# Optimization experiments

Measured on AMD Instinct MI355X. Metric: run time of the kernel, lower is better.

## Reference

```python
import jax, jax.numpy as jnp
import numpy as np

NV = 16384
NF = 32768
B = 4


def _build_laplacian(nv, nf, seed=0):
    # Faithful replication of the torch module's __init__ laplacian construction.
    rng = np.random.RandomState(seed)
    faces = rng.randint(0, nv, size=(nf, 3)).astype(np.int64)
    lap = np.zeros((nv, nv), dtype=np.float32)
    lap[faces[:, 0], faces[:, 1]] = -1
    lap[faces[:, 1], faces[:, 0]] = -1
    lap[faces[:, 1], faces[:, 2]] = -1
    lap[faces[:, 2], faces[:, 1]] = -1
    lap[faces[:, 2], faces[:, 0]] = -1
    lap[faces[:, 0], faces[:, 2]] = -1
    r, c = np.diag_indices(nv)
    lap[r, c] = -lap.sum(1)
    deg = lap[r, c]  # degree per vertex (>= 0)
    # vectorized version of: for i: if lap[i,i] > 0: lap[i,:] /= lap[i,i]
    scale = np.where(deg > 0, 1.0 / np.maximum(deg, 1.0), 1.0).astype(np.float32)
    lap = lap * scale[:, None]
    return lap


def setup_inputs() -> dict:
    key = jax.random.key(0)
    x = jax.random.normal(key, (B, NV, 3), dtype=jnp.float32)
    laplacian = jnp.asarray(_build_laplacian(NV, NF))
    return {"x": x, "laplacian": laplacian}


def reference(x, laplacian):
    # y[b, i, d] = sum_j L[i, j] * x[b, j, d]
    y = jnp.einsum("ij,bjd->bid", laplacian, x)
    # squared L2 norm per batch element (sum over all non-batch dims)
    loss = jnp.sum(y * y, axis=(1, 2))  # [B]
    return loss
```

## Files before the change

kernel.cpp:

```cpp
#include <hip/hip_runtime.h>

#define NV 16384
#define BROWS 32
#define JT 256
#define NT (NV / JT)
#define THREADS 256

typedef const __attribute__((address_space(1))) void* as1_ptr;
typedef __attribute__((address_space(3))) void* as3_ptr;

__device__ __forceinline__ void gload_lds16_nt(const float* g, float* l) {
  __builtin_amdgcn_global_load_lds((as1_ptr)g, (as3_ptr)l, 16, 0, 2);
}

#define FENCE asm volatile("" ::: "memory")
#define WAITV(n) asm volatile("s_waitcnt vmcnt(" #n ")" ::: "memory")

__global__ __launch_bounds__(THREADS, 2) void lap_loss_kernel(
    const float* __restrict__ x, const float* __restrict__ L,
    float* __restrict__ out) {
  __shared__ float lbuf[2][BROWS][JT];

  const int lane = threadIdx.x & 63;
  const int w    = threadIdx.x >> 6;
  const size_t i0 = (size_t)blockIdx.x * BROWS;

  const int phase = (int)(blockIdx.x & (NT - 1));

  const float* gL[8];
#pragma unroll
  for (int r = 0; r < 8; ++r)
    gL[r] = L + (i0 + 8 * w + r) * NV + lane * 4;

  const float* gx = x + (size_t)w * NV * 3 + lane * 12;

  float acc[BROWS][3];
#pragma unroll
  for (int r = 0; r < BROWS; ++r)
#pragma unroll
    for (int d = 0; d < 3; ++d) acc[r][d] = 0.f;

  const size_t j0 = (size_t)phase * JT;
  float4 xc0 = *(const float4*)(gx + j0 * 3 + 0);
  float4 xc1 = *(const float4*)(gx + j0 * 3 + 4);
  float4 xc2 = *(const float4*)(gx + j0 * 3 + 8);
  FENCE;
#pragma unroll
  for (int r = 0; r < 8; ++r)
    gload_lds16_nt(gL[r] + j0, &lbuf[0][8 * w + r][0]);
  FENCE;

#pragma unroll 1
  for (int t = 0; t < NT; ++t) {
    const int cur = t & 1;

    float4 xn0, xn1, xn2;
    if (t + 1 < NT) {
      const size_t jn = (size_t)((t + 1 + phase) & (NT - 1)) * JT;
#pragma unroll
      for (int r = 0; r < 8; ++r)
        gload_lds16_nt(gL[r] + jn, &lbuf[cur ^ 1][8 * w + r][0]);
      FENCE;
      const float* gxn = gx + jn * 3;
      xn0 = *(const float4*)(gxn + 0);
      xn1 = *(const float4*)(gxn + 4);
      xn2 = *(const float4*)(gxn + 8);
      FENCE;
      WAITV(11);
    } else {
      WAITV(0);
    }
    __builtin_amdgcn_s_barrier();
    FENCE;

    {
      const float xf[12] = {xc0.x, xc0.y, xc0.z, xc0.w,
                            xc1.x, xc1.y, xc1.z, xc1.w,
                            xc2.x, xc2.y, xc2.z, xc2.w};
#pragma unroll
      for (int r = 0; r < BROWS; ++r) {
        float4 lv = *(const float4*)&lbuf[cur][r][lane * 4];
        const float lf[4] = {lv.x, lv.y, lv.z, lv.w};
#pragma unroll
        for (int jj = 0; jj < 4; ++jj)
#pragma unroll
          for (int d = 0; d < 3; ++d)
            acc[r][d] = fmaf(lf[jj], xf[jj * 3 + d], acc[r][d]);
      }
    }

    FENCE;
    __builtin_amdgcn_s_barrier();
    FENCE;

    xc0 = xn0; xc1 = xn1; xc2 = xn2;
  }

  float s = 0.f;
#pragma unroll
  for (int r = 0; r < BROWS; ++r)
#pragma unroll
    for (int d = 0; d < 3; ++d) {
      float v = acc[r][d];
#pragma unroll
      for (int off = 32; off > 0; off >>= 1)
        v += __shfl_xor(v, off, 64);
      s += v * v;
    }

  if (lane == 0) atomicAdd(&out[w], s);
}

extern "C" void kernel_launch(void* const* d_in, const int* in_sizes, int n_in,
                              void* d_out, int out_size, void* d_ws, size_t ws_size,
                              hipStream_t stream) {
  const float* x = (const float*)d_in[0];
  const float* L = (const float*)d_in[1];
  float* out = (float*)d_out;

  hipMemsetAsync(out, 0, out_size * sizeof(float), stream);

  const int nblocks = NV / BROWS;
  lap_loss_kernel<<<nblocks, THREADS, 0, stream>>>(x, L, out);
}
```

Baseline: 196.6 us.

## Partition rows across waves instead of batches, each wave computes all batches

Each wave now owns 8 of the block's 32 Laplacian rows and computes all 4 batch columns, instead of every wave reading all 32 rows for its own batch. Each wave reads only its own slice of the shared L tile, cutting LDS read traffic fourfold. In exchange each wave loads all four batches' x values per tile (12 float4 loads instead of 3), which adds global/L2 traffic and register pressure. The vmcnt wait threshold is adjusted to match. Accumulator count per thread stays at 96.

New measurement: 389.9 us. 1.98x slower.

```diff
diff --git a/kernel.cpp b/kernel.cpp
--- a/kernel.cpp
+++ b/kernel.cpp
@@ -32,60 +32,69 @@
   for (int r = 0; r < 8; ++r)
     gL[r] = L + (i0 + 8 * w + r) * NV + lane * 4;
 
-  const float* gx = x + (size_t)w * NV * 3 + lane * 12;
+  const float* gx[4];
+#pragma unroll
+  for (int b = 0; b < 4; ++b) gx[b] = x + (size_t)b * NV * 3 + lane * 12;
 
-  float acc[BROWS][3];
+  float acc[8][4][3];
 #pragma unroll
-  for (int r = 0; r < BROWS; ++r)
+  for (int r = 0; r < 8; ++r)
 #pragma unroll
-    for (int d = 0; d < 3; ++d) acc[r][d] = 0.f;
+    for (int b = 0; b < 4; ++b)
+#pragma unroll
+      for (int d = 0; d < 3; ++d) acc[r][b][d] = 0.f;
+
+  float4 xc[4][3], xn[4][3];
 
   const size_t j0 = (size_t)phase * JT;
-  float4 xc0 = *(const float4*)(gx + j0 * 3 + 0);
-  float4 xc1 = *(const float4*)(gx + j0 * 3 + 4);
-  float4 xc2 = *(const float4*)(gx + j0 * 3 + 8);
-  FENCE;
 #pragma unroll
   for (int r = 0; r < 8; ++r)
     gload_lds16_nt(gL[r] + j0, &lbuf[0][8 * w + r][0]);
+  FENCE;
+#pragma unroll
+  for (int b = 0; b < 4; ++b) {
+    const float4* p = (const float4*)(gx[b] + j0 * 3);
+    xc[b][0] = p[0]; xc[b][1] = p[1]; xc[b][2] = p[2];
+  }
   FENCE;
 
 #pragma unroll 1
   for (int t = 0; t < NT; ++t) {
     const int cur = t & 1;
 
-    float4 xn0, xn1, xn2;
     if (t + 1 < NT) {
       const size_t jn = (size_t)((t + 1 + phase) & (NT - 1)) * JT;
 #pragma unroll
       for (int r = 0; r < 8; ++r)
         gload_lds16_nt(gL[r] + jn, &lbuf[cur ^ 1][8 * w + r][0]);
       FENCE;
-      const float* gxn = gx + jn * 3;
-      xn0 = *(const float4*)(gxn + 0);
-      xn1 = *(const float4*)(gxn + 4);
-      xn2 = *(const float4*)(gxn + 8);
+#pragma unroll
+      for (int b = 0; b < 4; ++b) {
+        const float4* p = (const float4*)(gx[b] + jn * 3);
+        xn[b][0] = p[0]; xn[b][1] = p[1]; xn[b][2] = p[2];
+      }
       FENCE;
-      WAITV(11);
+      WAITV(20);
     } else {
       WAITV(0);
     }
     __builtin_amdgcn_s_barrier();
     FENCE;
 
-    {
-      const float xf[12] = {xc0.x, xc0.y, xc0.z, xc0.w,
-                            xc1.x, xc1.y, xc1.z, xc1.w,
-                            xc2.x, xc2.y, xc2.z, xc2.w};
 #pragma unroll
-      for (int r = 0; r < BROWS; ++r) {
-        float4 lv = *(const float4*)&lbuf[cur][r][lane * 4];
-        const float lf[4] = {lv.x, lv.y, lv.z, lv.w};
+    for (int r = 0; r < 8; ++r) {
+      float4 lv = *(const float4*)&lbuf[cur][8 * w + r][lane * 4];
+      const float lf[4] = {lv.x, lv.y, lv.z, lv.w};
+#pragma unroll
+      for (int b = 0; b < 4; ++b) {
+        const float xf[12] = {xc[b][0].x, xc[b][0].y, xc[b][0].z, xc[b][0].w,
+                              xc[b][1].x, xc[b][1].y, xc[b][1].z, xc[b][1].w,
+                              xc[b][2].x, xc[b][2].y, xc[b][2].z, xc[b][2].w};
 #pragma unroll
         for (int jj = 0; jj < 4; ++jj)
 #pragma unroll
           for (int d = 0; d < 3; ++d)
-            acc[r][d] = fmaf(lf[jj], xf[jj * 3 + d], acc[r][d]);
+            acc[r][b][d] = fmaf(lf[jj], xf[jj * 3 + d], acc[r][b][d]);
       }
     }
 
@@ -93,22 +102,30 @@
     __builtin_amdgcn_s_barrier();
     FENCE;
 
-    xc0 = xn0; xc1 = xn1; xc2 = xn2;
+#pragma unroll
+    for (int b = 0; b < 4; ++b) {
+      xc[b][0] = xn[b][0]; xc[b][1] = xn[b][1]; xc[b][2] = xn[b][2];
+    }
   }
 
-  float s = 0.f;
+  float s[4] = {0.f, 0.f, 0.f, 0.f};
 #pragma unroll
-  for (int r = 0; r < BROWS; ++r)
+  for (int r = 0; r < 8; ++r)
 #pragma unroll
-    for (int d = 0; d < 3; ++d) {
-      float v = acc[r][d];
+    for (int b = 0; b < 4; ++b)
 #pragma unroll
-      for (int off = 32; off > 0; off >>= 1)
-        v += __shfl_xor(v, off, 64);
-      s += v * v;
-    }
+      for (int d = 0; d < 3; ++d) {
+        float v = acc[r][b][d];
+#pragma unroll
+        for (int off = 32; off > 0; off >>= 1)
+          v += __shfl_xor(v, off, 64);
+        s[b] += v * v;
+      }
 
-  if (lane == 0) atomicAdd(&out[w], s);
+  if (lane == 0) {
+#pragma unroll
+    for (int b = 0; b < 4; ++b) atomicAdd(&out[b], s[b]);
+  }
 }
 
 extern "C" void kernel_launch(void* const* d_in, const int* in_sizes, int n_in,
```
